# Kernel optimization log

Hardware: AMD Instinct MI355X
Metric: run time of the kernel (lower is better)

Reference implementation:

```python
import jax, jax.numpy as jnp
import numpy as np

H = 1024
L = 4

def _lstm_layer(xs, w_ih, w_hh, b):
    # xs: [B, T, in]; w_ih: [4H, in]; w_hh: [4H, H]; b: [4H] (b_ih + b_hh)
    xp = jnp.einsum('bti,gi->btg', xs, w_ih) + b  # [B, T, 4H]
    xp = jnp.swapaxes(xp, 0, 1)                   # [T, B, 4H]
    B = xs.shape[0]
    h0 = jnp.zeros((B, H), xs.dtype)
    c0 = jnp.zeros((B, H), xs.dtype)

    def step(carry, xp_t):
        h, c = carry
        gates = xp_t + h @ w_hh.T                 # [B, 4H]
        i, f, g, o = jnp.split(gates, 4, axis=-1)  # PyTorch gate order i,f,g,o
        i = jax.nn.sigmoid(i)
        f = jax.nn.sigmoid(f)
        g = jnp.tanh(g)
        o = jax.nn.sigmoid(o)
        c = f * c + i * g
        h = o * jnp.tanh(c)
        return (h, c), h

    (hT, cT), hs = jax.lax.scan(step, (h0, c0), xp)
    return jnp.swapaxes(hs, 0, 1), hT             # [B, T, H], [B, H]


def setup_inputs() -> dict:
    key = jax.random.key(0)
    ks = jax.random.split(key, 8)
    s = 1.0 / np.sqrt(H)
    u = lambda k, shp: jax.random.uniform(k, shp, jnp.float32, -s, s)
    return {
        'x': jax.random.normal(ks[0], (64, 256, 2), jnp.float32),
        'w_ih0': u(ks[1], (4 * H, 2)),            # layer 0 input weights
        'w_ih_rest': u(ks[2], (L - 1, 4 * H, H)), # layers 1..3 input weights
        'w_hh': u(ks[3], (L, 4 * H, H)),
        'b_ih': u(ks[4], (L, 4 * H)),
        'b_hh': u(ks[5], (L, 4 * H)),
        'fc_w': u(ks[6], (1, H)),
        'fc_b': u(ks[7], (1,)),
    }


def reference(x, w_ih0, w_ih_rest, w_hh, b_ih, b_hh, fc_w, fc_b):
    # 4-layer LSTM, batch_first, zero initial states; dropout inactive (eval mode).
    hs, hT = _lstm_layer(x, w_ih0, w_hh[0], b_ih[0] + b_hh[0])
    for l in range(1, L):
        hs, hT = _lstm_layer(hs, w_ih_rest[l - 1], w_hh[l], b_ih[l] + b_hh[l])
    # fc applied to final hidden state of last layer
    return hT @ fc_w.T + fc_b                      # [B, 1]
```

## Files before the change

kernel.cpp:

```cpp
#include <hip/hip_runtime.h>
#include <hip/hip_bf16.h>
#include <hip/hip_fp16.h>


#define H      1024
#define BATCH  64
#define T      256
#define RINGN  8

typedef _Float16 f16x8 __attribute__((ext_vector_type(8)));
typedef _Float16 f16x4 __attribute__((ext_vector_type(4)));
typedef float    f32x4 __attribute__((ext_vector_type(4)));

#define WPACK_HH_SZ  (4ull*64*32*4*64*8*2)
#define WPACK_IH_SZ  (3ull*64*32*4*64*8*2)
#define HRING_OFF    (WPACK_HH_SZ + WPACK_IH_SZ)
#define SLOT_ELEMS   65536
#define SLOT_BYTES   131072ull
#define CNT_INTS     (4*257*16)
#define CNT_BYTES    ((unsigned long long)CNT_INTS*4)

__host__ __device__ __forceinline__ unsigned long long ring_bytes(int nslot) {
  return 4ull*(unsigned)nslot*SLOT_BYTES;
}
__device__ __forceinline__ int cidx(int l, int s) { return (l*257 + s)*16; }
__device__ __forceinline__ int fidx(int l, int w) { return (l*64 + w)*16; }

__device__ __forceinline__ int aslot(int s, int fresh) {
  if (!fresh) return s & 7;
  return (s >= 256) ? 256 : (int)(__brev((unsigned)s) >> 24);
}

__device__ __forceinline__ void wait_eq64(int* p) {
  int it = 0;
  while (__hip_atomic_load(p, __ATOMIC_RELAXED, __HIP_MEMORY_SCOPE_AGENT) < 64) {
    __builtin_amdgcn_s_sleep(1);
    if (++it > 100000000) break;
  }
}

__device__ __forceinline__ void wait_ge(const int* p, int tgt) {
  int it = 0;
  while (__hip_atomic_load(p, __ATOMIC_RELAXED, __HIP_MEMORY_SCOPE_AGENT) < tgt) {
    __builtin_amdgcn_s_sleep(1);
    if (++it > 100000000) break;
  }
}

__device__ __forceinline__ f16x8 load_h8_sc(const _Float16* p) {
  const unsigned long long* q = (const unsigned long long*)p;
  unsigned long long lo = __hip_atomic_load(q,     __ATOMIC_RELAXED, __HIP_MEMORY_SCOPE_AGENT);
  unsigned long long hi = __hip_atomic_load(q + 1, __ATOMIC_RELAXED, __HIP_MEMORY_SCOPE_AGENT);
  union { unsigned long long u[2]; f16x8 v; } c;
  c.u[0] = lo; c.u[1] = hi;
  return c.v;
}

__global__ void pack_kernel(const float* __restrict__ w_ih_rest,
                            const float* __restrict__ w_hh,
                            char* __restrict__ ws, int nslot)
{
  const long long NS_HH = 4ll*64*32*4*64;
  const long long NS_IH = 3ll*64*32*4*64;
  const long long NS_HZ = 4ll*8192;
  const long long NTOT  = NS_HH + NS_IH + NS_HZ + 256;
  _Float16* whh_dst = (_Float16*)ws;
  _Float16* wih_dst = (_Float16*)(ws + WPACK_HH_SZ);
  int* cnt = (int*)(ws + HRING_OFF + ring_bytes(nslot));
  for (long long i = blockIdx.x*(long long)blockDim.x + threadIdx.x; i < NTOT;
       i += (long long)gridDim.x*blockDim.x) {
    if (i < NS_HH + NS_IH) {
      const bool is_hh = (i < NS_HH);
      long long slot = is_hh ? i : (i - NS_HH);
      long long j = slot;
      int lane = (int)(j & 63); j >>= 6;
      int nt   = (int)(j & 3);  j >>= 2;
      int ks   = (int)(j & 31); j >>= 5;
      int wg   = (int)(j & 63); j >>= 6;
      int l    = (int)j;
      int row = nt*1024 + wg*16 + (lane & 15);
      int col = ks*32 + (lane >> 4)*8;
      const float* src = (is_hh ? w_hh : w_ih_rest) + ((long long)l*4096 + row)*1024 + col;
      f16x8 v;
      #pragma unroll
      for (int e = 0; e < 8; e++) v[e] = (_Float16)src[e];
      *(f16x8*)((is_hh ? whh_dst : wih_dst) + slot*8) = v;
    } else if (i < NS_HH + NS_IH + NS_HZ) {
      long long j = i - (NS_HH + NS_IH);
      long long l = j >> 13;
      long long off = j & 8191;
      uint4 z = make_uint4(0,0,0,0);
      ((uint4*)(ws + HRING_OFF))[(l*(long long)nslot)*8192 + off] = z;
    } else {
      int k = (int)(i - (NS_HH + NS_IH + NS_HZ));
      cnt[k*16] = 0;
    }
  }
}

template <int NKS>
__global__ __launch_bounds__(256, 1) void lstm_main(
    const float* __restrict__ x,
    const float* __restrict__ wih0,
    const float* __restrict__ bih,
    const float* __restrict__ bhh,
    char* __restrict__ ws, int nslot, int fresh)
{
  __builtin_amdgcn_fence(__ATOMIC_ACQUIRE, "agent");

  extern __shared__ char lds[];
  _Float16* whh_lds = (_Float16*)lds;
  _Float16* bufs    = (_Float16*)(lds + (size_t)NKS*4096);

  const int l   = blockIdx.x >> 6;
  const int wg  = blockIdx.x & 63;
  const int tid = threadIdx.x;
  const int wave = tid >> 6;
  const int lane = tid & 63;

  const _Float16* wpack_hh = (const _Float16*)ws + (size_t)(l*64 + wg)*65536;
  const _Float16* wpack_ih = (l > 0)
      ? (const _Float16*)(ws + WPACK_HH_SZ) + (size_t)((l-1)*64 + wg)*65536
      : wpack_hh;
  _Float16* hring = (_Float16*)(ws + HRING_OFF);
  int* cnt  = (int*)(ws + HRING_OFF + ring_bytes(nslot));
  int* cnt2 = cnt + CNT_INTS;

  {
    const uint4* src = (const uint4*)wpack_hh;
    uint4* dst = (uint4*)whh_lds;
    for (int i = tid; i < NKS*256; i += 256) dst[i] = src[i];
  }

  const int b_ew = tid >> 2;
  const int u0   = (tid & 3) * 4;
  float cst[4] = {0.f, 0.f, 0.f, 0.f};
  float bias[4][4];
  float wx0[4][4], wx1[4][4];
  #pragma unroll
  for (int ii = 0; ii < 4; ii++) {
    #pragma unroll
    for (int g = 0; g < 4; g++) {
      int row = g*1024 + wg*16 + u0 + ii;
      bias[ii][g] = bih[l*4096 + row] + bhh[l*4096 + row];
      if (l == 0) { wx0[ii][g] = wih0[row*2]; wx1[ii][g] = wih0[row*2 + 1]; }
      else        { wx0[ii][g] = 0.f;         wx1[ii][g] = 0.f; }
    }
  }
  __syncthreads();

  const int m_row = lane & 15, quad = lane >> 4;

  for (int s = 1; s <= T; s++) {
    if (fresh) {
      if (l == 0) {
        if (lane < 16) wait_ge(cnt + fidx(0, wave*16 + lane), s - 1);
      } else {
        if (wave == 0)      { if (lane < 32) wait_ge(cnt + fidx(l-1, lane),      s); }
        else if (wave == 1) { if (lane < 32) wait_ge(cnt + fidx(l-1, 32 + lane), s); }
        else if (wave == 2) { if (lane < 32) wait_ge(cnt + fidx(l,   lane),      s - 1); }
        else                { if (lane < 32) wait_ge(cnt + fidx(l,   32 + lane), s - 1); }
      }
    } else {
      if (wave == 0) {
        wait_ge(cnt + fidx(l, lane), s - 1);
      } else if (wave == 1) {
        if (l > 0) wait_ge(cnt + fidx(l - 1, lane), s);
      } else if (tid == 128) {
        if (l < 3 && s > RINGN) wait_eq64(&cnt2[cidx(l, s-RINGN)]);
      }
      __syncthreads();
    }

    const _Float16* asrc = (l > 0 && wave < 2)
        ? hring + ((size_t)(l-1)*nslot + aslot(s,   fresh))*SLOT_ELEMS
        : hring + ((size_t)l*nslot     + aslot(s-1, fresh))*SLOT_ELEMS;

    f32x4 acc[4][4];
    #pragma unroll
    for (int mt = 0; mt < 4; mt++)
      #pragma unroll
      for (int nt = 0; nt < 4; nt++) acc[mt][nt] = (f32x4){0.f, 0.f, 0.f, 0.f};

    auto kb_lds = [&](int ks, bool plain) {
      const int kb = ks*32 + quad*8;
      f16x8 a[4], bb[4];
      #pragma unroll
      for (int mt = 0; mt < 4; mt++) {
        const _Float16* ap = asrc + (size_t)(mt*16 + m_row)*1024 + kb;
        a[mt] = plain ? *(const f16x8*)ap : load_h8_sc(ap);
      }
      #pragma unroll
      for (int nt = 0; nt < 4; nt++)
        bb[nt] = *(const f16x8*)(whh_lds + ((ks*4 + nt)*64 + lane)*8);
      #pragma unroll
      for (int mt = 0; mt < 4; mt++)
        #pragma unroll
        for (int nt = 0; nt < 4; nt++)
          acc[mt][nt] = __builtin_amdgcn_mfma_f32_16x16x32_f16(a[mt], bb[nt], acc[mt][nt], 0, 0, 0);
    };
    auto kb_glob = [&](int ks, const _Float16* bsrc, bool plain) {
      const int kb = ks*32 + quad*8;
      f16x8 a[4], bb[4];
      #pragma unroll
      for (int mt = 0; mt < 4; mt++) {
        const _Float16* ap = asrc + (size_t)(mt*16 + m_row)*1024 + kb;
        a[mt] = plain ? *(const f16x8*)ap : load_h8_sc(ap);
      }
      #pragma unroll
      for (int nt = 0; nt < 4; nt++)
        bb[nt] = *(const f16x8*)(bsrc + ((size_t)(ks*4 + nt)*64 + lane)*8);
      #pragma unroll
      for (int mt = 0; mt < 4; mt++)
        #pragma unroll
        for (int nt = 0; nt < 4; nt++)
          acc[mt][nt] = __builtin_amdgcn_mfma_f32_16x16x32_f16(a[mt], bb[nt], acc[mt][nt], 0, 0, 0);
    };

    const bool pl = (fresh != 0);
    if (l == 0) {
      if (NKS >= 32 || wave < 3) {
        #pragma unroll 4
        for (int i = 0; i < 8; i++) kb_lds(wave*8 + i, pl);
      } else {
        #pragma unroll 4
        for (int i = 0; i < 4; i++) kb_lds(24 + i, pl);
        #pragma unroll
        for (int i = 0; i < 4; i++) kb_glob(28 + i, wpack_hh, pl);
      }
    } else if (wave < 2) {
      #pragma unroll 4
      for (int i = 0; i < 16; i++) kb_glob(wave*16 + i, wpack_ih, pl);
    } else if (wave == 2) {
      #pragma unroll 4
      for (int i = 0; i < 16; i++) kb_lds(i, pl);
    } else {
      #pragma unroll 4
      for (int i = 0; i < (NKS - 16); i++) kb_lds(16 + i, pl);
      #pragma unroll
      for (int i = NKS - 16; i < 16; i++) kb_glob(16 + i, wpack_hh, pl);
    }

    {
      _Float16* mybuf = bufs + (size_t)wave*4096;
      #pragma unroll
      for (int mt = 0; mt < 4; mt++)
        #pragma unroll
        for (int nt = 0; nt < 4; nt++) {
          f16x4 v;
          #pragma unroll
          for (int e = 0; e < 4; e++) v[e] = (_Float16)acc[mt][nt][e];
          *(f16x4*)(mybuf + ((mt*4 + nt)*64 + lane)*4) = v;
        }
    }
    if (!fresh && tid == 0 && l > 0)
      __hip_atomic_fetch_add(&cnt2[cidx(l-1, s)], 1, __ATOMIC_RELAXED, __HIP_MEMORY_SCOPE_AGENT);
    __syncthreads();

    {
      const int mt = b_ew >> 4, q = (b_ew & 15) >> 2, reg = b_ew & 3;
      float xs0 = 0.f, xs1 = 0.f;
      if (l == 0) {
        xs0 = x[((size_t)b_ew*T + (s-1))*2];
        xs1 = x[((size_t)b_ew*T + (s-1))*2 + 1];
      }
      f16x4 hv;
      #pragma unroll
      for (int ii = 0; ii < 4; ii++) {
        const int u = u0 + ii;
        float pre[4];
        #pragma unroll
        for (int g = 0; g < 4; g++) {
          int idx = ((mt*4 + g)*64 + (u + 16*q))*4 + reg;
          pre[g] = (float)bufs[idx] + (float)bufs[4096 + idx]
                 + (float)bufs[8192 + idx] + (float)bufs[12288 + idx]
                 + bias[ii][g] + wx0[ii][g]*xs0 + wx1[ii][g]*xs1;
        }
        float ig = 1.f/(1.f + __expf(-pre[0]));
        float fg = 1.f/(1.f + __expf(-pre[1]));
        float gg = 2.f/(1.f + __expf(-2.f*pre[2])) - 1.f;
        float og = 1.f/(1.f + __expf(-pre[3]));
        float c  = fg*cst[ii] + ig*gg;
        cst[ii] = c;
        float th = 2.f/(1.f + __expf(-2.f*c)) - 1.f;
        hv[ii] = (_Float16)(og*th);
      }
      _Float16* hdst = hring + ((size_t)l*nslot + aslot(s, fresh))*SLOT_ELEMS
                     + (size_t)b_ew*1024 + wg*16 + u0;
      union { f16x4 v; unsigned long long u; } cv; cv.v = hv;
      __hip_atomic_store((unsigned long long*)hdst, cv.u,
                         __ATOMIC_RELAXED, __HIP_MEMORY_SCOPE_AGENT);
    }
    __syncthreads();
    if (tid == 0)
      __hip_atomic_store(cnt + fidx(l, wg), s,
                         __ATOMIC_RELAXED, __HIP_MEMORY_SCOPE_AGENT);
  }
}

__global__ void fc_kernel(const char* __restrict__ ws,
                          const float* __restrict__ fcw,
                          const float* __restrict__ fcb,
                          float* __restrict__ out, int nslot, int fresh)
{
  const _Float16* h3 = (const _Float16*)(ws + HRING_OFF)
                     + ((size_t)3*nslot + aslot(T, fresh))*SLOT_ELEMS;
  __shared__ float red[256];
  const int tid = threadIdx.x;
  const int b = tid >> 2, p = tid & 3;
  float sum = 0.f;
  for (int j = p*256; j < p*256 + 256; j++)
    sum += fcw[j] * (float)h3[(size_t)b*1024 + j];
  red[tid] = sum;
  __syncthreads();
  if (p == 0)
    out[b] = red[tid] + red[tid+1] + red[tid+2] + red[tid+3] + fcb[0];
}

extern "C" void kernel_launch(void* const* d_in, const int* in_sizes, int n_in,
                              void* d_out, int out_size, void* d_ws, size_t ws_size,
                              hipStream_t stream)
{
  const float* x    = (const float*)d_in[0];
  const float* wih0 = (const float*)d_in[1];
  const float* wihr = (const float*)d_in[2];
  const float* whh  = (const float*)d_in[3];
  const float* bih  = (const float*)d_in[4];
  const float* bhh  = (const float*)d_in[5];
  const float* fcw  = (const float*)d_in[6];
  const float* fcb  = (const float*)d_in[7];
  float* out = (float*)d_out;
  char* ws = (char*)d_ws;
  (void)in_sizes; (void)n_in; (void)out_size;

  const unsigned long long ws_big   = HRING_OFF + ring_bytes(257) + 2*CNT_BYTES;
  const unsigned long long ws_small = HRING_OFF + ring_bytes(8)   + 2*CNT_BYTES;
  if (ws_size < ws_small) return;
  const int fresh = (ws_size >= ws_big) ? 1 : 0;
  const int nslot = fresh ? 257 : 8;

  hipError_t eFull = hipFuncSetAttribute(
      reinterpret_cast<const void*>(lstm_main<32>),
      hipFuncAttributeMaxDynamicSharedMemorySize, 163840);
  if (eFull != hipSuccess)
    hipFuncSetAttribute(reinterpret_cast<const void*>(lstm_main<28>),
                        hipFuncAttributeMaxDynamicSharedMemorySize, 147456);

  hipMemsetAsync(ws + HRING_OFF + ring_bytes(nslot), 0, (size_t)(2*CNT_BYTES), stream);
  pack_kernel<<<512, 256, 0, stream>>>(wihr, whh, ws, nslot);
  if (eFull == hipSuccess)
    lstm_main<32><<<256, 256, 163840, stream>>>(x, wih0, bih, bhh, ws, nslot, fresh);
  else
    lstm_main<28><<<256, 256, 147456, stream>>>(x, wih0, bih, bhh, ws, nslot, fresh);
  fc_kernel<<<1, 256, 0, stream>>>(ws, fcw, fcb, out, nslot, fresh);
}
```

Before: 3.408 ms.

## Replace per-block end-of-step barrier with per-wave release flags

Each step now ends with every wave publishing its own progress counter (four ints per 64-byte line) using a release store, instead of a __syncthreads followed by a single store from thread 0. Waiters read all four per-wave counters with two 64-bit loads and require all of them to reach the target. An extra lane waits on its own block's counters to guard the block's local reuse. The aim is to drop a block-wide barrier from the recurrent critical path so a wave can signal as soon as its h stores are done. In exchange, spin loads get wider and the ordering logic is more delicate.

```diff
diff --git a/kernel.cpp b/kernel.cpp
--- a/kernel.cpp
+++ b/kernel.cpp
@@ -39,11 +39,17 @@
   }
 }
 
-__device__ __forceinline__ void wait_ge(const int* p, int tgt) {
+__device__ __forceinline__ void wait_all4_ge(const int* p, int tgt) {
+  const unsigned long long* q = (const unsigned long long*)p;
   int it = 0;
-  while (__hip_atomic_load(p, __ATOMIC_RELAXED, __HIP_MEMORY_SCOPE_AGENT) < tgt) {
+  for (;;) {
+    unsigned long long ab = __hip_atomic_load(q,     __ATOMIC_RELAXED, __HIP_MEMORY_SCOPE_AGENT);
+    unsigned long long cd = __hip_atomic_load(q + 1, __ATOMIC_RELAXED, __HIP_MEMORY_SCOPE_AGENT);
+    int a = (int)ab, b = (int)(ab >> 32);
+    int c = (int)cd, d = (int)(cd >> 32);
+    if (a >= tgt && b >= tgt && c >= tgt && d >= tgt) break;
     __builtin_amdgcn_s_sleep(1);
-    if (++it > 100000000) break;
+    if (++it > 50000000) break;
   }
 }
 
@@ -63,7 +69,7 @@
   const long long NS_HH = 4ll*64*32*4*64;
   const long long NS_IH = 3ll*64*32*4*64;
   const long long NS_HZ = 4ll*8192;
-  const long long NTOT  = NS_HH + NS_IH + NS_HZ + 256;
+  const long long NTOT  = NS_HH + NS_IH + NS_HZ + 1024;
   _Float16* whh_dst = (_Float16*)ws;
   _Float16* wih_dst = (_Float16*)(ws + WPACK_HH_SZ);
   int* cnt = (int*)(ws + HRING_OFF + ring_bytes(nslot));
@@ -92,8 +98,9 @@
       uint4 z = make_uint4(0,0,0,0);
       ((uint4*)(ws + HRING_OFF))[(l*(long long)nslot)*8192 + off] = z;
     } else {
-      int k = (int)(i - (NS_HH + NS_IH + NS_HZ));
-      cnt[k*16] = 0;
+      long long j = i - (NS_HH + NS_IH + NS_HZ);
+      int line = (int)(j >> 2), w = (int)(j & 3);
+      cnt[line*16 + w] = 0;
     }
   }
 }
@@ -154,18 +161,23 @@
   for (int s = 1; s <= T; s++) {
     if (fresh) {
       if (l == 0) {
-        if (lane < 16) wait_ge(cnt + fidx(0, wave*16 + lane), s - 1);
+        if (lane < 16)       wait_all4_ge(cnt + fidx(0, wave*16 + lane), s - 1);
+        else if (lane == 32) wait_all4_ge(cnt + fidx(0, wg), s - 1);
       } else {
-        if (wave == 0)      { if (lane < 32) wait_ge(cnt + fidx(l-1, lane),      s); }
-        else if (wave == 1) { if (lane < 32) wait_ge(cnt + fidx(l-1, 32 + lane), s); }
-        else if (wave == 2) { if (lane < 32) wait_ge(cnt + fidx(l,   lane),      s - 1); }
-        else                { if (lane < 32) wait_ge(cnt + fidx(l,   32 + lane), s - 1); }
+        if (wave == 0)      { if (lane < 32) wait_all4_ge(cnt + fidx(l-1, lane),      s);
+                              else if (lane == 32) wait_all4_ge(cnt + fidx(l, wg), s - 1); }
+        else if (wave == 1) { if (lane < 32) wait_all4_ge(cnt + fidx(l-1, 32 + lane), s);
+                              else if (lane == 32) wait_all4_ge(cnt + fidx(l, wg), s - 1); }
+        else if (wave == 2) { if (lane < 32) wait_all4_ge(cnt + fidx(l,   lane),      s - 1);
+                              else if (lane == 32) wait_all4_ge(cnt + fidx(l, wg), s - 1); }
+        else                { if (lane < 32) wait_all4_ge(cnt + fidx(l,   32 + lane), s - 1);
+                              else if (lane == 32) wait_all4_ge(cnt + fidx(l, wg), s - 1); }
       }
     } else {
       if (wave == 0) {
-        wait_ge(cnt + fidx(l, lane), s - 1);
+        wait_all4_ge(cnt + fidx(l, lane), s - 1);
       } else if (wave == 1) {
-        if (l > 0) wait_ge(cnt + fidx(l - 1, lane), s);
+        if (l > 0) wait_all4_ge(cnt + fidx(l - 1, lane), s);
       } else if (tid == 128) {
         if (l < 3 && s > RINGN) wait_eq64(&cnt2[cidx(l, s-RINGN)]);
       }
@@ -291,10 +303,20 @@
       __hip_atomic_store((unsigned long long*)hdst, cv.u,
                          __ATOMIC_RELAXED, __HIP_MEMORY_SCOPE_AGENT);
     }
-    __syncthreads();
-    if (tid == 0)
-      __hip_atomic_store(cnt + fidx(l, wg), s,
-                         __ATOMIC_RELAXED, __HIP_MEMORY_SCOPE_AGENT);
+
+    if (fresh) {
+      if (lane == 0)
+        __hip_atomic_store(cnt + fidx(l, wg) + wave, s,
+                           __ATOMIC_RELEASE, __HIP_MEMORY_SCOPE_AGENT);
+    } else {
+      __syncthreads();
+      if (tid == 0) {
+        __hip_atomic_store(cnt + fidx(l, wg) + 0, s, __ATOMIC_RELAXED, __HIP_MEMORY_SCOPE_AGENT);
+        __hip_atomic_store(cnt + fidx(l, wg) + 1, s, __ATOMIC_RELAXED, __HIP_MEMORY_SCOPE_AGENT);
+        __hip_atomic_store(cnt + fidx(l, wg) + 2, s, __ATOMIC_RELAXED, __HIP_MEMORY_SCOPE_AGENT);
+        __hip_atomic_store(cnt + fidx(l, wg) + 3, s, __ATOMIC_RELAXED, __HIP_MEMORY_SCOPE_AGENT);
+      }
+    }
   }
 }
 
```

After: 8.080 ms. +137.1%, slower.
